# Kernel optimization log

Measured on AMD Instinct MI355X. Metric: run time of the kernel, lower is better.

Reference implementation:

```python
import jax, jax.numpy as jnp
import numpy as np

DIM = 256
HEADS = 8
BS = 8
N = 1024
NEG = -1.0e9


def setup_inputs() -> dict:
    key = jax.random.key(0)
    ks = jax.random.split(key, 8)
    feats = jax.random.normal(ks[0], (BS, N, DIM), dtype=jnp.float32)
    adj_mat = (jax.random.uniform(ks[1], (BS, N, N)) < 0.1).astype(jnp.float32)
    s = 1.0 / np.sqrt(DIM)
    fc_w = jax.random.normal(ks[2], (DIM, DIM * HEADS), dtype=jnp.float32) * s
    fc_b = jnp.zeros((DIM * HEADS,), dtype=jnp.float32)
    q_w = jax.random.normal(ks[3], (DIM, 1), dtype=jnp.float32) * s
    q_b = jnp.zeros((1,), dtype=jnp.float32)
    k_w = jax.random.normal(ks[4], (DIM, 1), dtype=jnp.float32) * s
    k_b = jnp.zeros((1,), dtype=jnp.float32)
    fp_w = jax.random.normal(ks[5], (DIM * HEADS, DIM), dtype=jnp.float32) * (1.0 / np.sqrt(DIM * HEADS))
    fp_b = jnp.zeros((DIM,), dtype=jnp.float32)
    return {"feats": feats, "adj_mat": adj_mat, "fc_w": fc_w, "fc_b": fc_b,
            "q_w": q_w, "q_b": q_b, "k_w": k_w, "k_b": k_b,
            "fp_w": fp_w, "fp_b": fp_b}


def reference(feats, adj_mat, fc_w, fc_b, q_w, q_b, k_w, k_b, fp_w, fp_b):
    bs, n, dim = feats.shape
    # [bs, N, heads*dim] -> [bs, heads, N, dim]
    feat_proj = (feats @ fc_w + fc_b).reshape(bs, n, HEADS, dim).transpose(0, 2, 1, 3)
    q = feat_proj @ q_w + q_b            # [bs, heads, N, 1]
    k = feat_proj @ k_w + k_b            # [bs, heads, N, 1]
    logits = q + jnp.swapaxes(k, -1, -2)  # additive scores [bs, heads, N, N]
    masked = logits + (1.0 - adj_mat[:, None]) * NEG
    masked = jax.nn.leaky_relu(masked, negative_slope=0.01)
    attn = jax.nn.softmax(masked, axis=-1)  # dropout is identity at eval
    out = attn @ feat_proj                   # [bs, heads, N, dim]
    out = out.transpose(0, 2, 1, 3).reshape(bs, n, HEADS * dim)
    out = out @ fp_w + fp_b + feats          # residual=True
    return jax.nn.sigmoid(out)
```

## Files before the change

kernel.cpp:

```cpp
#include <hip/hip_runtime.h>
#include <hip/hip_bf16.h>

typedef unsigned short u16;
typedef unsigned int u32;
typedef unsigned long long u64;
typedef __attribute__((ext_vector_type(8))) short short8;
typedef __attribute__((ext_vector_type(4))) float floatx4;
typedef const __attribute__((address_space(1))) void* gp_t;
typedef __attribute__((address_space(3))) void* sp_t;

#define LOG2E 1.44269504088896f

static __device__ __forceinline__ float exp2_raw(float x) {
    float r; asm("v_exp_f32 %0, %1" : "=v"(r) : "v"(x)); return r;
}

static __device__ __forceinline__ u16 f2bf(float x) {
    __hip_bfloat16 h = __float2bfloat16(x);
    union { __hip_bfloat16 h; u16 u; } cv; cv.h = h; return cv.u;
}

__global__ __launch_bounds__(256)
void k_prepall(const float* __restrict__ feats, const float* __restrict__ adj,
               const float* __restrict__ fc_w, const float* __restrict__ fc_b,
               const float* __restrict__ q_w, const float* __restrict__ q_b,
               const float* __restrict__ k_w, const float* __restrict__ k_b,
               const float* __restrict__ fp_w,
               u16* __restrict__ feats2, u16* __restrict__ maskH,
               u16* __restrict__ fcw2, u16* __restrict__ fpw2,
               u16* __restrict__ W, float* __restrict__ C) {
    __shared__ float shbuf[64 * 65];
    int id = blockIdx.x, t = threadIdx.x;
    if (id < 2048) {
        long g = (long)id * 256 + t;
        const float4* ap = (const float4*)adj + g * 4;
        u32 mm = 0;
        #pragma unroll
        for (int w = 0; w < 4; w++) {
            float4 f = ap[w];
            mm |= (f.x > 0.f ? 1u : 0u) << (4 * w);
            mm |= (f.y > 0.f ? 1u : 0u) << (4 * w + 1);
            mm |= (f.z > 0.f ? 1u : 0u) << (4 * w + 2);
            mm |= (f.w > 0.f ? 1u : 0u) << (4 * w + 3);
        }
        maskH[g] = (u16)mm;
    } else if (id < 3072) {
        int n = (id - 2048) * 8 + (t >> 5), c = t & 31;
        const float* src = feats + (long)n * 256 + c * 8;
        float4 f0 = *(const float4*)src, f1 = *(const float4*)(src + 4);
        u16 tmp[8] = {f2bf(f0.x), f2bf(f0.y), f2bf(f0.z), f2bf(f0.w),
                      f2bf(f1.x), f2bf(f1.y), f2bf(f1.z), f2bf(f1.w)};
        *(int4*)&feats2[(long)c * 65536 + n * 8] = *(int4*)tmp;
    } else if (id < 3200) {
        int b = id - 3072, bx = b & 31, by = b >> 5;
        float (*tt)[65] = (float(*)[65])shbuf;
        int c = t & 63, r0 = t >> 6;
        for (int rr = r0; rr < 64; rr += 4)
            tt[rr][c] = fc_w[(long)(by * 64 + rr) * 2048 + bx * 64 + c];
        __syncthreads();
        int hdl = t & 63;
        #pragma unroll
        for (int oo = 0; oo < 2; oo++) {
            int o = (t >> 6) + oo * 4;
            u16 tmp[8];
            #pragma unroll
            for (int e = 0; e < 8; e++) tmp[e] = f2bf(tt[o * 8 + e][hdl]);
            *(int4*)&fcw2[(long)(by * 8 + o) * 16384 + (bx * 64 + hdl) * 8] = *(int4*)tmp;
        }
    } else if (id < 3328) {
        int b = id - 3200, bx = b & 3, by = b >> 2;
        float (*tt)[65] = (float(*)[65])shbuf;
        int c = t & 63, r0 = t >> 6;
        for (int rr = r0; rr < 64; rr += 4)
            tt[rr][c] = fp_w[(long)(by * 64 + rr) * 256 + bx * 64 + c];
        __syncthreads();
        int cl = t & 63;
        #pragma unroll
        for (int oo = 0; oo < 2; oo++) {
            int o = (t >> 6) + oo * 4;
            u16 tmp[8];
            #pragma unroll
            for (int e = 0; e < 8; e++) tmp[e] = f2bf(tt[o * 8 + e][cl]);
            *(int4*)&fpw2[(long)(by * 8 + o) * 2048 + (bx * 64 + cl) * 8] = *(int4*)tmp;
        }
    } else {
        int t2 = id - 3328, x = t2 & 15, dq = t2 >> 4;
        int h = x & 7, kind = x >> 3;
        const float* w = kind ? k_w : q_w;
        float* ws_ = shbuf;
        ws_[t] = w[t];
        __syncthreads();
        int wave = t >> 6, lane = t & 63;
        for (int j = 0; j < 16; j++) {
            int d = dq * 64 + wave * 16 + j;
            const float* row = fc_w + (long)d * 2048 + h * 256;
            float a = row[lane]        * ws_[lane]
                    + row[64 + lane]   * ws_[64 + lane]
                    + row[128 + lane]  * ws_[128 + lane]
                    + row[192 + lane]  * ws_[192 + lane];
            #pragma unroll
            for (int o = 1; o < 64; o <<= 1) a += __shfl_xor(a, o);
            if (lane == 0) W[(long)x * 256 + d] = f2bf(a);
        }
        if (dq == 0) {
            float cv = fc_b[h * 256 + t] * ws_[t];
            float* cred = shbuf + 256;
            cred[t] = cv;
            __syncthreads();
            if (t < 64) {
                float s = cred[t] + cred[t + 64] + cred[t + 128] + cred[t + 192];
                #pragma unroll
                for (int o = 1; o < 64; o <<= 1) s += __shfl_xor(s, o);
                if (t == 0) C[x] = s + (kind ? k_b[0] : q_b[0]);
            }
        }
    }
}

__global__ __launch_bounds__(256)
void k_g1qk(const u16* __restrict__ fcw2, const u16* __restrict__ feats2,
            const float* __restrict__ bias, u16* __restrict__ V2,
            const u16* __restrict__ Wb, const float* __restrict__ C,
            float* __restrict__ qo, float* __restrict__ ko) {
    __shared__ u16 smem[16896];
    int tid = threadIdx.x, wave = tid >> 6, lane = tid & 63;
    int q = lane >> 4, n16 = lane & 15;

    if (blockIdx.y >= 16) {
        int blk = (blockIdx.y - 16) * 64 + blockIdx.x;
        int rowBase = blk * 64 + wave * 16;
        floatx4 acc = {};
        #pragma unroll
        for (int k0 = 0; k0 < 256; k0 += 32) {
            short8 af = *(const short8*)&feats2[(long)((k0 >> 3) + q) * 65536
                                                + (rowBase + n16) * 8];
            short8 bf = *(const short8*)&Wb[n16 * 256 + k0 + q * 8];
            acc = __builtin_amdgcn_mfma_f32_16x16x32_bf16(af, bf, acc, 0, 0, 0);
        }
        float cc = C[n16];
        #pragma unroll
        for (int r = 0; r < 4; r++) {
            int gr = rowBase + q * 4 + r;
            int b = gr >> 10, nn = gr & 1023;
            float v = (acc[r] + cc) * LOG2E;
            if (n16 < 8) qo[((b * 8 + n16) << 10) + nn] = v;
            else         ko[((b * 8 + (n16 - 8)) << 10) + nn] = v;
        }
        return;
    }

    int rowBase = blockIdx.y * 128;
    int colBase = blockIdx.x * 128;
    int wr = wave >> 1, wc = wave & 1;
    floatx4 acc[4][4] = {};

    auto dma = [&](int k0, int p) {
        int kc = k0 >> 3;
        u16* Ab = smem + p * 4096;
        u16* Bb = smem + 8192 + p * 4096;
        #pragma unroll
        for (int r = 0; r < 2; r++) {
            __builtin_amdgcn_global_load_lds(
                (gp_t)&fcw2[(long)(kc + wave) * 16384 + (rowBase + r * 64 + lane) * 8],
                (sp_t)&Ab[(wave * 128 + r * 64 + lane) * 8], 16, 0, 0);
            __builtin_amdgcn_global_load_lds(
                (gp_t)&feats2[(long)(kc + wave) * 65536 + (colBase + r * 64 + lane) * 8],
                (sp_t)&Bb[(wave * 128 + r * 64 + lane) * 8], 16, 0, 0);
        }
    };

    dma(0, 0);
    __syncthreads();
    for (int k0 = 0; k0 < 256; k0 += 32) {
        int p = (k0 >> 5) & 1;
        u16* Ab = smem + p * 4096;
        u16* Bb = smem + 8192 + p * 4096;
        short8 af[4], bfr[4];
        #pragma unroll
        for (int i = 0; i < 4; i++)
            af[i] = *(short8*)&Ab[(q * 128 + wr * 64 + i * 16 + n16) * 8];
        #pragma unroll
        for (int i = 0; i < 4; i++)
            bfr[i] = *(short8*)&Bb[(q * 128 + wc * 64 + i * 16 + n16) * 8];
        if (k0 + 32 < 256) dma(k0 + 32, p ^ 1);
        #pragma unroll
        for (int mi = 0; mi < 4; mi++)
            #pragma unroll
            for (int ni = 0; ni < 4; ni++)
                acc[mi][ni] = __builtin_amdgcn_mfma_f32_16x16x32_bf16(
                    af[mi], bfr[ni], acc[mi][ni], 0, 0, 0);
        __syncthreads();
    }

    u16* eb = smem;
    #pragma unroll
    for (int mi = 0; mi < 4; mi++) {
        #pragma unroll
        for (int r = 0; r < 4; r++) {
            int d_loc = wr * 64 + mi * 16 + q * 4 + r;
            float bv = bias[rowBase + d_loc];
            #pragma unroll
            for (int ni = 0; ni < 4; ni++) {
                int nn_loc = wc * 64 + ni * 16 + n16;
                eb[d_loc * 132 + nn_loc] = f2bf(acc[mi][ni][r] + bv);
            }
        }
    }
    __syncthreads();
    int hB = rowBase >> 8, dB = rowBase & 255;
    int bB = colBase >> 10, cB = (colBase & 1023) >> 3;
    long vbase = ((long)(bB * 8 + hB)) << 18;
    #pragma unroll
    for (int j = 0; j < 8; j++) {
        int idx = j * 256 + tid;
        int dl = idx & 127, c8 = idx >> 7;
        *(int4*)&V2[vbase + (long)(cB + c8) * 2048 + (dB + dl) * 8]
            = *(int4*)&eb[dl * 132 + c8 * 8];
    }
}

__global__ __launch_bounds__(512)
__attribute__((amdgpu_waves_per_eu(4)))
void k_attn(const u32* __restrict__ maskW, const float* __restrict__ qv,
            const float* __restrict__ kv, const u16* __restrict__ fpjT2,
            u16* __restrict__ outh2) {
    __shared__ u16 smem[26624];
    __shared__ float qS[128], kS[1024], lsumS[512], rlS[128];

    int z = blockIdx.x;
    int b = z >> 3, h = z & 7;
    int i0 = blockIdx.y * 128;
    int tid = threadIdx.x;
    int wave = tid >> 6, lane = tid & 63;
    int wr = wave >> 2, wc = wave & 3;
    int q  = lane >> 4, n16 = lane & 15;

    if (tid < 256) *(float4*)&kS[tid * 4] = *(const float4*)&kv[(z << 10) + tid * 4];
    if (tid >= 256 && tid < 384) qS[tid - 256] = qv[(z << 10) + i0 + (tid - 256)];

    floatx4 acc[4][4] = {};
    int ar = tid >> 2;
    int jq = (tid & 3) * 8;
    const u32* mrow = maskW + (((long)(b << 10) + i0 + ar) << 5);
    const u16* Vbase = fpjT2 + ((long)z << 18);
    float lsum = 0.f;

    auto dma_v = [&](int k0, int p) {
        u16* Bb = smem + 10240 + p * 8192;
        #pragma unroll
        for (int t = 0; t < 2; t++) {
            int s = wave * 2 + t;
            __builtin_amdgcn_global_load_lds(
                (gp_t)&Vbase[((k0 >> 3) + (s >> 2)) * 2048 + ((s & 3) * 64 + lane) * 8],
                (sp_t)&Bb[((s >> 2) * 256 + (s & 3) * 64 + lane) * 8],
                16, 0, 0);
        }
    };

    __syncthreads();
    float qi = qS[ar];

    auto stage_p = [&](int p, u32 mw, float4 kA, float4 kB) {
        u16* Ab = smem + p * 5120;
        float kk[8] = {kA.x, kA.y, kA.z, kA.w, kB.x, kB.y, kB.z, kB.w};
        u32 pw[4];
        #pragma unroll
        for (int e2 = 0; e2 < 4; e2++) {
            float s0 = qi + kk[2 * e2];
            s0 = fmaxf(s0, 0.01f * s0);
            float p0 = ((mw >> (2 * e2)) & 1u) ? exp2_raw(s0) : 0.f;
            float s1 = qi + kk[2 * e2 + 1];
            s1 = fmaxf(s1, 0.01f * s1);
            float p1 = ((mw >> (2 * e2 + 1)) & 1u) ? exp2_raw(s1) : 0.f;
            lsum += p0 + p1;
            pw[e2] = __builtin_amdgcn_perm(__float_as_uint(p1), __float_as_uint(p0),
                                           0x07060302);
        }
        *(int4*)&Ab[ar * 40 + jq] = *(int4*)&pw[0];
    };

    {
        u32 mw0 = mrow[0] >> jq;
        float4 kA0 = *(const float4*)&kS[jq];
        float4 kB0 = *(const float4*)&kS[jq + 4];
        dma_v(0, 0);
        stage_p(0, mw0, kA0, kB0);
    }
    __syncthreads();

    for (int k0 = 0; k0 < 1024; k0 += 32) {
        int p = (k0 >> 5) & 1;
        u16* Ab = smem + p * 5120;
        u16* Bb = smem + 10240 + p * 8192;
        int kn = (k0 + 32 < 1024) ? k0 + 32 : 0;
        u32 mw = mrow[kn >> 5] >> jq;
        float4 kA = *(const float4*)&kS[kn + jq];
        float4 kB = *(const float4*)&kS[kn + jq + 4];
        short8 af[4], bfr[4];
        #pragma unroll
        for (int i = 0; i < 4; i++)
            af[i] = *(short8*)&Ab[(wr * 64 + i * 16 + n16) * 40 + q * 8];
        #pragma unroll
        for (int i = 0; i < 4; i++)
            bfr[i] = *(short8*)&Bb[(q * 256 + wc * 64 + i * 16 + n16) * 8];
        if (k0 + 32 < 1024) {
            dma_v(k0 + 32, p ^ 1);
            stage_p(p ^ 1, mw, kA, kB);
        }
        #pragma unroll
        for (int mi = 0; mi < 4; mi++)
            #pragma unroll
            for (int ni = 0; ni < 4; ni++)
                acc[mi][ni] = __builtin_amdgcn_mfma_f32_16x16x32_bf16(
                    af[mi], bfr[ni], acc[mi][ni], 0, 0, 0);
        __syncthreads();
    }

    lsumS[tid] = lsum;
    __syncthreads();
    if (tid < 128) {
        float l = lsumS[4 * tid] + lsumS[4 * tid + 1] +
                  lsumS[4 * tid + 2] + lsumS[4 * tid + 3];
        rlS[tid] = l > 0.f ? 1.f / l : 0.f;
    }
    __syncthreads();

    u16* eb = smem;
    long rowG = (long)(b * 1024 + i0);
    #pragma unroll
    for (int hh = 0; hh < 2; hh++) {
        if ((wc >> 1) == hh) {
            #pragma unroll
            for (int mi = 0; mi < 4; mi++) {
                #pragma unroll
                for (int r = 0; r < 4; r++) {
                    int grow = wr * 64 + mi * 16 + q * 4 + r;
                    float s = rlS[grow];
                    #pragma unroll
                    for (int ni = 0; ni < 4; ni++) {
                        int col = (wc & 1) * 64 + ni * 16 + n16;
                        eb[grow * 132 + col] = f2bf(acc[mi][ni][r] * s);
                    }
                }
            }
        }
        __syncthreads();
        #pragma unroll
        for (int j = 0; j < 4; j++) {
            int idx = j * 512 + tid;
            int row = idx & 127, c8 = idx >> 7;
            int chunk = h * 32 + hh * 16 + c8;
            *(int4*)&outh2[((long)chunk << 16) + (rowG + row) * 8]
                = *(int4*)&eb[row * 132 + c8 * 8];
        }
        __syncthreads();
    }
}

__global__ __launch_bounds__(256)
void k_g3(const u16* __restrict__ A2,
          const u16* __restrict__ B2,
          const float* __restrict__ bias,
          const float* __restrict__ resid,
          float* __restrict__ out) {
    __shared__ u16 As[2][16 * 64 * 8];
    __shared__ u16 Bs[2][16 * 32 * 8];
    int rowBase = blockIdx.x * 64;
    int colBase = blockIdx.y * 32;
    int tid = threadIdx.x, wave = tid >> 6, lane = tid & 63;
    int q = lane >> 4, n16 = lane & 15;
    floatx4 acc[2] = {};

    auto dma = [&](int k0, int p) {
        int kc = k0 >> 3;
        #pragma unroll
        for (int t = 0; t < 4; t++) {
            int c = wave + t * 4;
            __builtin_amdgcn_global_load_lds(
                (gp_t)&A2[(long)(kc + c) * 65536 + (rowBase + lane) * 8],
                (sp_t)&As[p][(c * 64 + lane) * 8], 16, 0, 0);
        }
        #pragma unroll
        for (int t = 0; t < 2; t++) {
            int c = wave * 2 + (lane >> 5) + t * 8;
            __builtin_amdgcn_global_load_lds(
                (gp_t)&B2[(long)(kc + c) * 2048 + (colBase + (lane & 31)) * 8],
                (sp_t)&Bs[p][(c * 32 + (lane & 31)) * 8], 16, 0, 0);
        }
    };

    dma(0, 0);
    __syncthreads();
    for (int k0 = 0; k0 < 2048; k0 += 128) {
        int p = (k0 >> 7) & 1;
        short8 af[4], bfr[4][2];
        #pragma unroll
        for (int kf = 0; kf < 4; kf++) {
            af[kf] = *(short8*)&As[p][((kf * 4 + q) * 64 + wave * 16 + n16) * 8];
            #pragma unroll
            for (int nf = 0; nf < 2; nf++)
                bfr[kf][nf] = *(short8*)&Bs[p][((kf * 4 + q) * 32 + nf * 16 + n16) * 8];
        }
        if (k0 + 128 < 2048) dma(k0 + 128, p ^ 1);
        #pragma unroll
        for (int kf = 0; kf < 4; kf++)
            #pragma unroll
            for (int nf = 0; nf < 2; nf++)
                acc[nf] = __builtin_amdgcn_mfma_f32_16x16x32_bf16(
                    af[kf], bfr[kf][nf], acc[nf], 0, 0, 0);
        __syncthreads();
    }

    #pragma unroll
    for (int nf = 0; nf < 2; nf++) {
        #pragma unroll
        for (int r = 0; r < 4; r++) {
            int grow = rowBase + wave * 16 + q * 4 + r;
            int gcol = colBase + nf * 16 + n16;
            float v = acc[nf][r] + bias[gcol] + resid[(long)grow * 256 + gcol];
            out[(long)grow * 256 + gcol] = 1.f / (1.f + __expf(-v));
        }
    }
}

extern "C" void kernel_launch(void* const* d_in, const int* in_sizes, int n_in,
                              void* d_out, int out_size, void* d_ws, size_t ws_size,
                              hipStream_t stream) {
    const float* feats = (const float*)d_in[0];
    const float* adj   = (const float*)d_in[1];
    const float* fc_w  = (const float*)d_in[2];
    const float* fc_b  = (const float*)d_in[3];
    const float* q_w   = (const float*)d_in[4];
    const float* q_b   = (const float*)d_in[5];
    const float* k_w   = (const float*)d_in[6];
    const float* k_b   = (const float*)d_in[7];
    const float* fp_w  = (const float*)d_in[8];
    const float* fp_b  = (const float*)d_in[9];

    char* ws = (char*)d_ws;
    u16*   feats2 = (u16*)ws;   ws += (size_t)2097152 * 2;
    u16*   fcw2   = (u16*)ws;   ws += (size_t)524288 * 2;
    u16*   fpw2   = (u16*)ws;   ws += (size_t)524288 * 2;
    u16*   fpjT2  = (u16*)ws;   ws += (size_t)16777216 * 2;
    float* qv     = (float*)ws; ws += (size_t)65536 * 4;
    float* kv     = (float*)ws; ws += (size_t)65536 * 4;
    u16*   outh2  = (u16*)ws;   ws += (size_t)16777216 * 2;
    u64*   maskB  = (u64*)ws;   ws += (size_t)131072 * 8;
    u16*   Weff   = (u16*)ws;   ws += (size_t)4096 * 2;
    float* Ceff   = (float*)ws; ws += (size_t)16 * 4;

    k_prepall<<<3392, 256, 0, stream>>>(feats, adj, fc_w, fc_b, q_w, q_b,
                                        k_w, k_b, fp_w,
                                        feats2, (u16*)maskB, fcw2, fpw2, Weff, Ceff);

    k_g1qk<<<dim3(64, 18), 256, 0, stream>>>(fcw2, feats2, fc_b, fpjT2,
                                             Weff, Ceff, qv, kv);

    k_attn<<<dim3(64, 8), 512, 0, stream>>>((const u32*)maskB, qv, kv, fpjT2, outh2);

    k_g3<<<dim3(128, 8), 256, 0, stream>>>(outh2, fpw2, fp_b, feats, (float*)d_out);
}
```

Baseline: 192.6 us.

## Compute softmax row sums via MFMA with ones vector; shrink g3 K-tile

The attention kernel no longer accumulates row sums in scalar code followed by a shared-memory reduction. It issues an extra MFMA per row tile against a bf16 ones column, so the row sums come out of the matrix unit using the same bf16-rounded probabilities as the numerator. Separately, the output-projection GEMM halves its K step from 128 to 64, halving its LDS buffers and issuing more loop iterations with more barriers. The extra MFMAs add about 25% matrix work in the attention loop, in exchange for removing VALU adds and a reduction pass.

```diff
diff --git a/kernel.cpp b/kernel.cpp
--- a/kernel.cpp
+++ b/kernel.cpp
@@ -225,7 +225,7 @@
             const float* __restrict__ kv, const u16* __restrict__ fpjT2,
             u16* __restrict__ outh2) {
     __shared__ u16 smem[26624];
-    __shared__ float qS[128], kS[1024], lsumS[512], rlS[128];
+    __shared__ float qS[128], kS[1024], rlS[128];
 
     int z = blockIdx.x;
     int b = z >> 3, h = z & 7;
@@ -239,11 +239,16 @@
     if (tid >= 256 && tid < 384) qS[tid - 256] = qv[(z << 10) + i0 + (tid - 256)];
 
     floatx4 acc[4][4] = {};
+    floatx4 acc_rs[4] = {};
+    union { short8 v; u32 w[4]; } uo;
+    u32 ob = (n16 == 0) ? 0x3F803F80u : 0u;
+    uo.w[0] = ob; uo.w[1] = ob; uo.w[2] = ob; uo.w[3] = ob;
+    short8 onesf = uo.v;
+
     int ar = tid >> 2;
     int jq = (tid & 3) * 8;
     const u32* mrow = maskW + (((long)(b << 10) + i0 + ar) << 5);
     const u16* Vbase = fpjT2 + ((long)z << 18);
-    float lsum = 0.f;
 
     auto dma_v = [&](int k0, int p) {
         u16* Bb = smem + 10240 + p * 8192;
@@ -272,7 +277,6 @@
             float s1 = qi + kk[2 * e2 + 1];
             s1 = fmaxf(s1, 0.01f * s1);
             float p1 = ((mw >> (2 * e2 + 1)) & 1u) ? exp2_raw(s1) : 0.f;
-            lsum += p0 + p1;
             pw[e2] = __builtin_amdgcn_perm(__float_as_uint(p1), __float_as_uint(p0),
                                            0x07060302);
         }
@@ -308,20 +312,26 @@
             stage_p(p ^ 1, mw, kA, kB);
         }
         #pragma unroll
-        for (int mi = 0; mi < 4; mi++)
+        for (int mi = 0; mi < 4; mi++) {
             #pragma unroll
             for (int ni = 0; ni < 4; ni++)
                 acc[mi][ni] = __builtin_amdgcn_mfma_f32_16x16x32_bf16(
                     af[mi], bfr[ni], acc[mi][ni], 0, 0, 0);
-        __syncthreads();
-    }
-
-    lsumS[tid] = lsum;
-    __syncthreads();
-    if (tid < 128) {
-        float l = lsumS[4 * tid] + lsumS[4 * tid + 1] +
-                  lsumS[4 * tid + 2] + lsumS[4 * tid + 3];
-        rlS[tid] = l > 0.f ? 1.f / l : 0.f;
+            acc_rs[mi] = __builtin_amdgcn_mfma_f32_16x16x32_bf16(
+                af[mi], onesf, acc_rs[mi], 0, 0, 0);
+        }
+        __syncthreads();
+    }
+
+    if (wc == 0 && n16 == 0) {
+        #pragma unroll
+        for (int mi = 0; mi < 4; mi++)
+            #pragma unroll
+            for (int r = 0; r < 4; r++) {
+                int grow = wr * 64 + mi * 16 + q * 4 + r;
+                float l = acc_rs[mi][r];
+                rlS[grow] = l > 0.f ? 1.f / l : 0.f;
+            }
     }
     __syncthreads();
 
@@ -363,8 +373,8 @@
           const float* __restrict__ bias,
           const float* __restrict__ resid,
           float* __restrict__ out) {
-    __shared__ u16 As[2][16 * 64 * 8];
-    __shared__ u16 Bs[2][16 * 32 * 8];
+    __shared__ u16 As[2][8 * 64 * 8];
+    __shared__ u16 Bs[2][8 * 32 * 8];
     int rowBase = blockIdx.x * 64;
     int colBase = blockIdx.y * 32;
     int tid = threadIdx.x, wave = tid >> 6, lane = tid & 63;
@@ -374,36 +384,33 @@
     auto dma = [&](int k0, int p) {
         int kc = k0 >> 3;
         #pragma unroll
-        for (int t = 0; t < 4; t++) {
+        for (int t = 0; t < 2; t++) {
             int c = wave + t * 4;
             __builtin_amdgcn_global_load_lds(
                 (gp_t)&A2[(long)(kc + c) * 65536 + (rowBase + lane) * 8],
                 (sp_t)&As[p][(c * 64 + lane) * 8], 16, 0, 0);
         }
-        #pragma unroll
-        for (int t = 0; t < 2; t++) {
-            int c = wave * 2 + (lane >> 5) + t * 8;
-            __builtin_amdgcn_global_load_lds(
-                (gp_t)&B2[(long)(kc + c) * 2048 + (colBase + (lane & 31)) * 8],
-                (sp_t)&Bs[p][(c * 32 + (lane & 31)) * 8], 16, 0, 0);
-        }
+        __builtin_amdgcn_global_load_lds(
+            (gp_t)&B2[(long)(kc + wave * 2 + (lane >> 5)) * 2048
+                      + (colBase + (lane & 31)) * 8],
+            (sp_t)&Bs[p][(wave * 64 + lane) * 8], 16, 0, 0);
     };
 
     dma(0, 0);
     __syncthreads();
-    for (int k0 = 0; k0 < 2048; k0 += 128) {
-        int p = (k0 >> 7) & 1;
-        short8 af[4], bfr[4][2];
-        #pragma unroll
-        for (int kf = 0; kf < 4; kf++) {
+    for (int k0 = 0; k0 < 2048; k0 += 64) {
+        int p = (k0 >> 6) & 1;
+        short8 af[2], bfr[2][2];
+        #pragma unroll
+        for (int kf = 0; kf < 2; kf++) {
             af[kf] = *(short8*)&As[p][((kf * 4 + q) * 64 + wave * 16 + n16) * 8];
             #pragma unroll
             for (int nf = 0; nf < 2; nf++)
                 bfr[kf][nf] = *(short8*)&Bs[p][((kf * 4 + q) * 32 + nf * 16 + n16) * 8];
         }
-        if (k0 + 128 < 2048) dma(k0 + 128, p ^ 1);
-        #pragma unroll
-        for (int kf = 0; kf < 4; kf++)
+        if (k0 + 64 < 2048) dma(k0 + 64, p ^ 1);
+        #pragma unroll
+        for (int kf = 0; kf < 2; kf++)
             #pragma unroll
             for (int nf = 0; nf < 2; nf++)
                 acc[nf] = __builtin_amdgcn_mfma_f32_16x16x32_bf16(
```

Result: slower. 262.5 us (+36.3%).
